# Kernel optimization log

Measured on AMD Instinct MI355X. Metric: run time of the kernel, lower is better.

The kernel has to match this reference:

```python
import jax, jax.numpy as jnp
import numpy as np

N_FFT = 256
HOP = 64            # fft_stride
WIN_LEN = 1024      # window_length (samples)
STRIDE = 256        # MPF window stride (samples)
FS = 2000.0
BANDS = [(0.0, 25.0), (25.0, 50.0), (50.0, 100.0), (100.0, 200.0), (200.0, 400.0), (400.0, 1000.0)]


def setup_inputs() -> dict:
    key = jax.random.key(0)
    x = jax.random.normal(key, (8, 32, 16000), dtype=jnp.float32)
    return {"inputs": x}


def _mpf_forward(inputs):
    # --- channelwise STFT (center=False, onesided, hann periodic=False) ---
    window = jnp.asarray(np.hanning(N_FFT), dtype=inputs.dtype)  # matches torch.hann_window(periodic=False)
    wnorm = jnp.linalg.norm(window)
    B, C, T = inputs.shape
    n_frames = 1 + (T - N_FFT) // HOP
    fidx = np.arange(n_frames)[:, None] * HOP + np.arange(N_FFT)[None, :]
    frames = inputs[..., fidx]                       # (B, C, n_frames, n_fft)
    spec = jnp.fft.rfft(frames * window, axis=-1) / wnorm  # (B, C, n_frames, F)
    spec = jnp.swapaxes(spec, -1, -2)                # (B, C, F, n_frames)

    # --- sliding window over STFT frames ---
    size = WIN_LEN // HOP   # 16
    step = STRIDE // HOP    # 4
    n_win = (n_frames - size) // step + 1
    widx = np.arange(n_win)[:, None] * step + np.arange(size)[None, :]
    win = spec[..., widx]                            # (B, C, F, n_win, size)
    x = jnp.transpose(win, (0, 3, 2, 1, 4))          # (B, n_win, F, C, size)

    # --- cross-spectral density: X X^H / size, then |.|^2 ---
    csd = jnp.einsum('btfcw,btfdw->btfcd', x, jnp.conj(x)) / size
    csd = csd.real ** 2 + csd.imag ** 2              # (B, n_win, F, C, C) real

    # --- average FFT bins into frequency bands ---
    freqs = np.fft.rfftfreq(N_FFT, d=1.0 / FS)
    masks_np = np.stack([(freqs > lo) & (freqs <= hi) for lo, hi in BANDS]).astype(np.float32)
    masks = jnp.asarray(masks_np, dtype=csd.dtype)   # (n_bands, F)
    banded = jnp.einsum('btfcd,kf->btkcd', csd, masks) / masks.sum(axis=1)[None, None, :, None, None]

    # --- SPD matrix log via eigh, eigvals floored at 100*eps ---
    eigvals, eigvecs = jnp.linalg.eigh(banded)
    floor = 100.0 * jnp.finfo(banded.dtype).eps
    log_vals = jnp.log(jnp.maximum(eigvals, floor))
    out = jnp.einsum('...ij,...j,...kj->...ik', eigvecs, log_vals, eigvecs)

    # (batch, time, bands, c1, c2) -> (batch, bands, c1, c2, time)
    return jnp.transpose(out, (0, 2, 3, 4, 1))


def reference(inputs) -> jnp.ndarray:
    return _mpf_forward(inputs)
```

## Files before the change

### kernel.cpp

```cpp
#include <hip/hip_runtime.h>
#include <cstddef>

#define NFRM 247
#define NBIN 128
#define NC   32
#define NWIN 58
#define NMAT (8 * NWIN * 6)
#define NBT  (8 * NWIN)

__global__ __launch_bounds__(128) void k_stft(const float* __restrict__ x,
                                              float2* __restrict__ spec) {
  const int gid = (blockIdx.x & 7) * 7904 + (blockIdx.x >> 3);
  const int fr  = gid % NFRM;
  const int bc  = gid / NFRM;
  const int tid = threadIdx.x;

  __shared__ float  xw[256];
  __shared__ float2 Y[256];

  const float* xp = x + ((size_t)bc * 16000 + (size_t)fr * 64);

  #pragma unroll
  for (int k = 0; k < 2; ++k) {
    const int t = tid + k * 128;
    const float wv = 0.5f - 0.5f * __cosf((float)t * 0.024639942f);
    xw[t] = xp[t] * wv * 0.10226200f;
  }
  __syncthreads();

  #pragma unroll
  for (int k = 0; k < 2; ++k) {
    const int e = tid + k * 128;
    const int f0 = e >> 4, t0 = e & 15;
    float sA, cA;
    __sincosf((float)f0 * 0.39269908f, &sA, &cA);
    float wr = 1.f, wi = 0.f, re = 0.f, im = 0.f;
    #pragma unroll
    for (int t1 = 0; t1 < 16; ++t1) {
      const float v = xw[(t1 << 4) + t0];
      re = fmaf(v, wr, re);
      im = fmaf(v, wi, im);
      const float nwr = fmaf(wi, sA, wr * cA);
      const float nwi = fmaf(-wr, sA, wi * cA);
      wr = nwr; wi = nwi;
    }
    Y[e] = make_float2(re, im);
  }
  __syncthreads();

  const int f = tid + 1;
  const int f0 = f & 15;
  float sB, cB;
  __sincosf((float)f * 0.024543693f, &sB, &cB);
  float wr = 1.f, wi = 0.f, re = 0.f, im = 0.f;
  #pragma unroll
  for (int t0 = 0; t0 < 16; ++t0) {
    const float2 yv = Y[(f0 << 4) + t0];
    re += yv.x * wr - yv.y * wi;
    im += yv.x * wi + yv.y * wr;
    const float nwr = fmaf(wi, sB, wr * cB);
    const float nwi = fmaf(-wr, sB, wi * cB);
    wr = nwr; wi = nwi;
  }
  const int b = bc >> 5, c = bc & 31;
  spec[(((size_t)b * NFRM + fr) * NBIN + (f - 1)) * NC + c] = make_float2(re, im);
}

__global__ __launch_bounds__(256) void k_csd(const float2* __restrict__ spec,
                                             float* __restrict__ part) {
  const int bt  = (blockIdx.x & 7) * 58 + (blockIdx.x >> 3);
  const int p   = blockIdx.y;
  const int b   = bt / NWIN, t = bt % NWIN;
  const int tid = threadIdx.x;
  const int wv  = tid >> 6;
  const int lane = tid & 63;
  const int i0 = (lane >> 3) * 4;
  const int j0 = (lane & 7) * 4;

  __shared__ __align__(16) float2 rng[4][2][512];

  float bacc[16];
  #pragma unroll
  for (int e = 0; e < 16; ++e) bacc[e] = 0.f;

  const float2* sb = spec + (size_t)b * NFRM * NBIN * NC;
  const int fbase = 1 + 64 * p + 16 * wv;
  int slot = p ? (9 + wv) : (wv == 0 ? 0 : wv == 1 ? 4 : wv == 2 ? 6 : 7);

  #define BANDOF(f) ((f) <= 3 ? 0 : (f) <= 6 ? 1 : (f) <= 12 ? 2 : (f) <= 25 ? 3 : (f) <= 51 ? 4 : 5)
  int curband = BANDOF(fbase);

  #define FLUSH()                                                                \
    {                                                                            \
      float scl_;                                                                \
      switch (curband) {                                                         \
        case 0: case 1: scl_ = 1.f / 768.f;   break;                             \
        case 2:         scl_ = 1.f / 1536.f;  break;                             \
        case 3:         scl_ = 1.f / 3328.f;  break;                             \
        case 4:         scl_ = 1.f / 6656.f;  break;                             \
        default:        scl_ = 1.f / 19712.f; break;                             \
      }                                                                          \
      float* op_ = part + ((size_t)slot * NBT + bt) * 1024;                      \
      _Pragma("unroll")                                                          \
      for (int a = 0; a < 4; ++a)                                                \
        *(float4*)(op_ + (i0 + a) * 32 + j0) =                                   \
          make_float4(bacc[a * 4 + 0] * scl_, bacc[a * 4 + 1] * scl_,            \
                      bacc[a * 4 + 2] * scl_, bacc[a * 4 + 3] * scl_);           \
      _Pragma("unroll")                                                          \
      for (int e = 0; e < 16; ++e) bacc[e] = 0.f;                                \
    }

  #define STG_LOAD(itl, dst)                                                     \
    {                                                                            \
      const int f_ = fbase + (itl);                                              \
      const float2* fp_ = sb + (size_t)(f_ - 1) * NC;                            \
      _Pragma("unroll")                                                          \
      for (int r = 0; r < 8; ++r) {                                              \
        const int e_ = lane + r * 64;                                            \
        dst[r] = fp_[(size_t)(t * 4 + (e_ >> 5)) * (NBIN * NC) + (e_ & 31)];     \
      }                                                                          \
    }

  {
    float2 stg[8];
    STG_LOAD(0, stg)
    #pragma unroll
    for (int r = 0; r < 8; ++r) rng[wv][0][lane + r * 64] = stg[r];
  }

  #pragma unroll 1
  for (int itl = 0; itl < 16; ++itl) {
    float2 stg2[8];
    if (itl + 1 < 16) STG_LOAD(itl + 1, stg2)

    const int f = fbase + itl;
    if (f == 4 || f == 7 || f == 13 || f == 26 || f == 52) {
      FLUSH()
      ++slot;
      curband = BANDOF(f);
    }

    const float2* Xs = rng[wv][itl & 1];

    float accRe[16], accIm[16];
    #pragma unroll
    for (int e = 0; e < 16; ++e) { accRe[e] = 0.f; accIm[e] = 0.f; }

    #pragma unroll
    for (int s = 0; s < 16; ++s) {
      float2 xi[4], xj[4];
      #pragma unroll
      for (int a = 0; a < 4; ++a) {
        xi[a] = Xs[s * 32 + i0 + a];
        xj[a] = Xs[s * 32 + j0 + a];
      }
      #pragma unroll
      for (int a = 0; a < 4; ++a)
        #pragma unroll
        for (int d = 0; d < 4; ++d) {
          const int e = a * 4 + d;
          accRe[e] = fmaf(xi[a].x, xj[d].x, fmaf(xi[a].y, xj[d].y, accRe[e]));
          accIm[e] = fmaf(xi[a].y, xj[d].x, fmaf(-xi[a].x, xj[d].y, accIm[e]));
        }
    }

    #pragma unroll
    for (int e = 0; e < 16; ++e)
      bacc[e] = fmaf(accRe[e], accRe[e], fmaf(accIm[e], accIm[e], bacc[e]));

    if (itl + 1 < 16) {
      #pragma unroll
      for (int r = 0; r < 8; ++r) rng[wv][(itl + 1) & 1][lane + r * 64] = stg2[r];
    }
  }
  FLUSH()
  #undef STG_LOAD
  #undef FLUSH
  #undef BANDOF
}

__global__ __launch_bounds__(64) void k_eig(const float* __restrict__ part,
                                            float* __restrict__ eigTmp) {
  const int blk  = blockIdx.x;
  const int lane = threadIdx.x;
  const int h    = lane >> 5;
  const int c    = lane & 31;

  const int kq = blk % 6;
  const int bt = blk / 6;
  const int s0  = (kq <= 2) ? kq : (kq == 3 ? 3 : kq == 4 ? 5 : 8);
  const int cnt = (kq <= 2) ? 1  : (kq == 3 ? 2 : kq == 4 ? 3 : 5);

  __shared__ float sA[32][36];
  __shared__ float sSc[32];

  for (int u = lane; u < 1024; u += 64) {
    float s = 0.f;
    for (int q = 0; q < cnt; ++q)
      s += part[((size_t)(s0 + q) * NBT + bt) * 1024 + u];
    sA[u >> 5][u & 31] = s;
  }
  __syncthreads();

  float g[16];
  #pragma unroll
  for (int i = 0; i < 16; ++i) g[i] = sA[16 * h + i][c];

  float n;
  {
    float p0 = 0.f, p1 = 0.f, p2 = 0.f, p3 = 0.f;
    #pragma unroll
    for (int e = 0; e < 16; e += 4) {
      p0 = fmaf(g[e + 0], g[e + 0], p0);
      p1 = fmaf(g[e + 1], g[e + 1], p1);
      p2 = fmaf(g[e + 2], g[e + 2], p2);
      p3 = fmaf(g[e + 3], g[e + 3], p3);
    }
    const float pp = (p0 + p1) + (p2 + p3);
    const float op = __shfl_xor(pp, 32);
    n = h ? (op + pp) : (pp + op);
  }

  const float EPS2 = 1e-6f;
  #pragma unroll 1
  for (int sweep = 0; sweep < 10; ++sweep) {
    int anybad = 0;
    #pragma unroll 1
    for (int m = 1; m < 32; ++m) {
      const int pidx = (lane ^ m) << 2;
      float tmp[16];
      #pragma unroll
      for (int e = 0; e < 16; ++e)
        tmp[e] = __int_as_float(__builtin_amdgcn_ds_bpermute(pidx, __float_as_int(g[e])));
      const float np = __int_as_float(__builtin_amdgcn_ds_bpermute(pidx, __float_as_int(n)));

      float d0 = 0.f, d1 = 0.f, d2 = 0.f, d3 = 0.f;
      #pragma unroll
      for (int e = 0; e < 16; e += 4) {
        d0 = fmaf(g[e + 0], tmp[e + 0], d0);
        d1 = fmaf(g[e + 1], tmp[e + 1], d1);
        d2 = fmaf(g[e + 2], tmp[e + 2], d2);
        d3 = fmaf(g[e + 3], tmp[e + 3], d3);
      }
      const float pp = (d0 + d1) + (d2 + d3);
      const float op = __shfl_xor(pp, 32);
      const float bpq = h ? (op + pp) : (pp + op);

      const int bad = (bpq * bpq > EPS2 * n * np);
      anybad |= bad;
      if (bad) {
        const float tau = (np - n) * 0.5f * __builtin_amdgcn_rcpf(bpq);
        float tf = __builtin_amdgcn_rcpf(fabsf(tau) + __builtin_amdgcn_sqrtf(fmaf(tau, tau, 1.f)));
        if (tau < 0.f) tf = -tf;
        const float cr = __builtin_amdgcn_rsqf(fmaf(tf, tf, 1.f));
        const float sg = -tf * cr;
        n = fmaf(-tf, bpq, n);
        #pragma unroll
        for (int e = 0; e < 16; ++e) g[e] = fmaf(sg, tmp[e], cr * g[e]);
      }
    }
    if (!__any(anybad)) break;
  }

  float nx;
  {
    float p0 = 0.f, p1 = 0.f, p2 = 0.f, p3 = 0.f;
    #pragma unroll
    for (int e = 0; e < 16; e += 4) {
      p0 = fmaf(g[e + 0], g[e + 0], p0);
      p1 = fmaf(g[e + 1], g[e + 1], p1);
      p2 = fmaf(g[e + 2], g[e + 2], p2);
      p3 = fmaf(g[e + 3], g[e + 3], p3);
    }
    const float pp = (p0 + p1) + (p2 + p3);
    const float op = __shfl_xor(pp, 32);
    nx = h ? (op + pp) : (pp + op);
  }
  const float lv = 0.5f * __logf(fmaxf(nx, 1.4210855e-10f));
  const float sc = (nx > 1e-32f) ? (lv * __builtin_amdgcn_rcpf(nx)) : 0.f;

  __syncthreads();
  #pragma unroll
  for (int i = 0; i < 16; ++i) sA[c][16 * h + i] = g[i];
  if (h == 0) sSc[c] = sc;
  __syncthreads();

  float a[32];
  #pragma unroll
  for (int e = 0; e < 32; ++e) a[e] = sSc[e] * sA[e][c];

  float* ob = eigTmp + ((size_t)blk * 1024 + c * 32 + 16 * h);
  #pragma unroll
  for (int q = 0; q < 4; ++q) {
    float4 acc = make_float4(0.f, 0.f, 0.f, 0.f);
    #pragma unroll
    for (int e = 0; e < 32; ++e) {
      const float4 gv = *(const float4*)&sA[e][16 * h + 4 * q];
      acc.x = fmaf(a[e], gv.x, acc.x);
      acc.y = fmaf(a[e], gv.y, acc.y);
      acc.z = fmaf(a[e], gv.z, acc.z);
      acc.w = fmaf(a[e], gv.w, acc.w);
    }
    *(float4*)(ob + 4 * q) = acc;
  }
}

__global__ __launch_bounds__(256) void k_tr(const float* __restrict__ eigTmp,
                                            float* __restrict__ out) {
  const int bk    = blockIdx.x >> 3;
  const int chunk = blockIdx.x & 7;
  const int b = bk / 6, k = bk % 6;
  const int ij0 = chunk * 128;
  const int tid = threadIdx.x;

  __shared__ float tile[128 * 59];

  for (int u = tid; u < 128 * NWIN; u += 256) {
    const int t = u >> 7, ijl = u & 127;
    tile[ijl * 59 + t] = eigTmp[((size_t)(b * NWIN + t) * 6 + k) * 1024 + ij0 + ijl];
  }
  __syncthreads();

  float* ob = out + ((size_t)bk * 1024 + ij0) * NWIN;
  for (int u = tid; u < 128 * NWIN; u += 256) {
    ob[u] = tile[(u / NWIN) * 59 + (u % NWIN)];
  }
}

extern "C" void kernel_launch(void* const* d_in, const int* in_sizes, int n_in,
                              void* d_out, int out_size, void* d_ws, size_t ws_size,
                              hipStream_t stream) {
  const float* x = (const float*)d_in[0];
  float* outp = (float*)d_out;

  const size_t SPEC_B = (size_t)8 * NFRM * NBIN * NC * sizeof(float2);

  float2* spec   = (float2*)d_ws;
  float*  part   = (float*)((char*)d_ws + SPEC_B);
  float*  eigTmp = (float*)d_ws;

  k_stft<<<dim3(8 * 32 * NFRM), dim3(128), 0, stream>>>(x, spec);
  k_csd <<<dim3(NBT, 2),        dim3(256), 0, stream>>>(spec, part);
  k_eig <<<dim3(NMAT),          dim3(64),  0, stream>>>(part, eigTmp);
  k_tr  <<<dim3(48 * 8),        dim3(256), 0, stream>>>(eigTmp, outp);
}
```

Baseline: 424.2 us.

## Batch STFT over 32 channels per block for coalesced spectrum writes

The STFT kernel now assigns one (batch, frame) pair per 256-thread block and loops over four groups of 8 channels. The window is precomputed once per block, and the spectrum is written with adjacent threads covering adjacent channels, so stores to the channel-innermost layout are contiguous. Before, each block handled a single channel and wrote float2 values strided by 32 elements. The grid shrinks from about 63k tiny blocks to about 2k larger ones, with more shared memory and more syncs per block. The CSD kernel also gains a min-blocks-per-CU hint on its launch bounds.

```diff
diff --git a/kernel.cpp b/kernel.cpp
--- a/kernel.cpp
+++ b/kernel.cpp
@@ -8,66 +8,82 @@
 #define NMAT (8 * NWIN * 6)
 #define NBT  (8 * NWIN)
 
-__global__ __launch_bounds__(128) void k_stft(const float* __restrict__ x,
+__global__ __launch_bounds__(256) void k_stft(const float* __restrict__ x,
                                               float2* __restrict__ spec) {
-  const int gid = (blockIdx.x & 7) * 7904 + (blockIdx.x >> 3);
-  const int fr  = gid % NFRM;
-  const int bc  = gid / NFRM;
+  const int bid = blockIdx.x;
+  const int b   = bid & 7;
+  const int fr  = bid >> 3;
   const int tid = threadIdx.x;
 
-  __shared__ float  xw[256];
-  __shared__ float2 Y[256];
-
-  const float* xp = x + ((size_t)bc * 16000 + (size_t)fr * 64);
-
-  #pragma unroll
-  for (int k = 0; k < 2; ++k) {
-    const int t = tid + k * 128;
-    const float wv = 0.5f - 0.5f * __cosf((float)t * 0.024639942f);
-    xw[t] = xp[t] * wv * 0.10226200f;
-  }
-  __syncthreads();
-
-  #pragma unroll
-  for (int k = 0; k < 2; ++k) {
-    const int e = tid + k * 128;
-    const int f0 = e >> 4, t0 = e & 15;
-    float sA, cA;
-    __sincosf((float)f0 * 0.39269908f, &sA, &cA);
-    float wr = 1.f, wi = 0.f, re = 0.f, im = 0.f;
-    #pragma unroll
-    for (int t1 = 0; t1 < 16; ++t1) {
-      const float v = xw[(t1 << 4) + t0];
-      re = fmaf(v, wr, re);
-      im = fmaf(v, wi, im);
-      const float nwr = fmaf(wi, sA, wr * cA);
-      const float nwi = fmaf(-wr, sA, wi * cA);
-      wr = nwr; wi = nwi;
-    }
-    Y[e] = make_float2(re, im);
-  }
-  __syncthreads();
-
-  const int f = tid + 1;
-  const int f0 = f & 15;
-  float sB, cB;
-  __sincosf((float)f * 0.024543693f, &sB, &cB);
-  float wr = 1.f, wi = 0.f, re = 0.f, im = 0.f;
-  #pragma unroll
-  for (int t0 = 0; t0 < 16; ++t0) {
-    const float2 yv = Y[(f0 << 4) + t0];
-    re += yv.x * wr - yv.y * wi;
-    im += yv.x * wi + yv.y * wr;
-    const float nwr = fmaf(wi, sB, wr * cB);
-    const float nwi = fmaf(-wr, sB, wi * cB);
-    wr = nwr; wi = nwi;
-  }
-  const int b = bc >> 5, c = bc & 31;
-  spec[(((size_t)b * NFRM + fr) * NBIN + (f - 1)) * NC + c] = make_float2(re, im);
-}
-
-__global__ __launch_bounds__(256) void k_csd(const float2* __restrict__ spec,
-                                             float* __restrict__ part) {
+  __shared__ float w[256];
+  __shared__ float xw[8][257];
+  __shared__ float Yre[8][273];
+  __shared__ float Yim[8][273];
+
+  w[tid] = (0.5f - 0.5f * __cosf((float)tid * 0.024639942f)) * 0.10226200f;
+
+  float2* ob = spec + ((size_t)b * NFRM + fr) * (NBIN * NC);
+  const float* xb = x + ((size_t)b * 32) * 16000 + fr * 64;
+
+  for (int g = 0; g < 4; ++g) {
+    __syncthreads();
+    #pragma unroll
+    for (int k = 0; k < 8; ++k) {
+      const int u = tid + k * 256;
+      const int ch = u >> 8, t = u & 255;
+      xw[ch][t] = xb[(size_t)(g * 8 + ch) * 16000 + t] * w[t];
+    }
+    __syncthreads();
+
+    #pragma unroll
+    for (int k = 0; k < 8; ++k) {
+      const int u = tid + k * 256;
+      const int ch = u >> 8;
+      const int e = u & 255;
+      const int f0 = e >> 4, t0 = e & 15;
+      float sA, cA;
+      __sincosf((float)f0 * 0.39269908f, &sA, &cA);
+      float wr = 1.f, wi = 0.f, re = 0.f, im = 0.f;
+      #pragma unroll
+      for (int t1 = 0; t1 < 16; ++t1) {
+        const float v = xw[ch][(t1 << 4) + t0];
+        re = fmaf(v, wr, re);
+        im = fmaf(v, wi, im);
+        const float nwr = fmaf(wi, sA, wr * cA);
+        const float nwi = fmaf(-wr, sA, wi * cA);
+        wr = nwr; wi = nwi;
+      }
+      Yre[ch][e] = re;
+      Yim[ch][e] = im;
+    }
+    __syncthreads();
+
+    #pragma unroll
+    for (int q = 0; q < 4; ++q) {
+      const int j = tid + q * 256;
+      const int ch = j & 7;
+      const int f = (j >> 3) + 1;
+      const int f0 = f & 15;
+      float sB, cB;
+      __sincosf((float)f * 0.024543693f, &sB, &cB);
+      float wr = 1.f, wi = 0.f, re = 0.f, im = 0.f;
+      #pragma unroll
+      for (int t0 = 0; t0 < 16; ++t0) {
+        const float yr = Yre[ch][(f0 << 4) + t0];
+        const float yi = Yim[ch][(f0 << 4) + t0];
+        re += yr * wr - yi * wi;
+        im += yr * wi + yi * wr;
+        const float nwr = fmaf(wi, sB, wr * cB);
+        const float nwi = fmaf(-wr, sB, wi * cB);
+        wr = nwr; wi = nwi;
+      }
+      ob[(size_t)(f - 1) * NC + g * 8 + ch] = make_float2(re, im);
+    }
+  }
+}
+
+__global__ __launch_bounds__(256, 4) void k_csd(const float2* __restrict__ spec,
+                                                float* __restrict__ part) {
   const int bt  = (blockIdx.x & 7) * 58 + (blockIdx.x >> 3);
   const int p   = blockIdx.y;
   const int b   = bt / NWIN, t = bt % NWIN;
@@ -339,8 +355,8 @@
   float*  part   = (float*)((char*)d_ws + SPEC_B);
   float*  eigTmp = (float*)d_ws;
 
-  k_stft<<<dim3(8 * 32 * NFRM), dim3(128), 0, stream>>>(x, spec);
-  k_csd <<<dim3(NBT, 2),        dim3(256), 0, stream>>>(spec, part);
-  k_eig <<<dim3(NMAT),          dim3(64),  0, stream>>>(part, eigTmp);
-  k_tr  <<<dim3(48 * 8),        dim3(256), 0, stream>>>(eigTmp, outp);
-}
+  k_stft<<<dim3(8 * NFRM),  dim3(256), 0, stream>>>(x, spec);
+  k_csd <<<dim3(NBT, 2),    dim3(256), 0, stream>>>(spec, part);
+  k_eig <<<dim3(NMAT),      dim3(64),  0, stream>>>(part, eigTmp);
+  k_tr  <<<dim3(48 * 8),    dim3(256), 0, stream>>>(eigTmp, outp);
+}
```

Result: slower. 1.455 ms (+243.0%).
